# Optimization experiments

Hardware: AMD Instinct MI355X
Metric: run time of the kernel (lower is better)

## Reference

```python
import jax, jax.numpy as jnp
import numpy as np

V = 32000   # target_vocab_size
E = 512     # embedding_dim
L = 2       # enc_lstm_layers
HD = 512    # enc_lstm_hidden_dim (bidirectional encoder)
H = 2 * HD  # decoder LSTM hidden size
B = 16
T = 128
BOS = 1
CTX = L * 2 * HD          # stepwise context dim = 2048
IN0 = E + CTX             # decoder LSTM layer-0 input dim = 2560


def setup_inputs() -> dict:
    key = jax.random.key(0)
    ks = jax.random.split(key, 12)
    def w(k, shape, fan_in):
        return jax.random.normal(k, shape, jnp.float32) * np.float32(1.0 / np.sqrt(fan_in))
    return {
        "enc_lstm_hidden": jax.random.normal(ks[0], (2 * L, B, HD), jnp.float32),
        "enc_lstm_ctxt": jax.random.normal(ks[1], (2 * L, B, HD), jnp.float32),
        "minibatch_target": jax.random.randint(ks[2], (B, T), 0, V, dtype=jnp.int32),
        "emb": w(ks[3], (V, E), E),
        "w_ih_0": w(ks[4], (4 * H, IN0), IN0),
        "w_hh_0": w(ks[5], (4 * H, H), H),
        "b_ih_0": jnp.zeros((4 * H,), jnp.float32),
        "b_hh_0": jnp.zeros((4 * H,), jnp.float32),
        "w_ih_1": w(ks[6], (4 * H, H), H),
        "w_hh_1": w(ks[7], (4 * H, H), H),
        "b_ih_1": jnp.zeros((4 * H,), jnp.float32),
        "b_hh_1": jnp.zeros((4 * H,), jnp.float32),
        "fc_w": w(ks[8], (V, H), H),
        "fc_b": jnp.zeros((V,), jnp.float32),
    }


def _lstm_layer(x_seq, h0, c0, w_ih, w_hh, b):
    """x_seq: [T, B, in]; returns top outputs [T, B, H]. torch gate order i,f,g,o."""
    def step(carry, x):
        h, c = carry
        g = x @ w_ih.T + h @ w_hh.T + b
        i, f, gg, o = jnp.split(g, 4, axis=-1)
        c = jax.nn.sigmoid(f) * c + jax.nn.sigmoid(i) * jnp.tanh(gg)
        h = jax.nn.sigmoid(o) * jnp.tanh(c)
        return (h, c), h
    (hT, cT), ys = jax.lax.scan(step, (h0, c0), x_seq)
    return ys, hT, cT


def reference(enc_lstm_hidden, enc_lstm_ctxt, minibatch_target, emb,
              w_ih_0, w_hh_0, b_ih_0, b_hh_0,
              w_ih_1, w_hh_1, b_ih_1, b_hh_1, fc_w, fc_b):
    # _reshape_encoder_state: [2L,B,HD] -> [L,B,2HD] (interleave fwd/bwd per layer)
    def reshape_state(s):
        return s.reshape(L, 2, B, HD).transpose(0, 2, 1, 3).reshape(L, B, 2 * HD)
    h0 = reshape_state(enc_lstm_hidden)
    c0 = reshape_state(enc_lstm_ctxt)
    # stepwise input context: [B, 2L*HD]
    ctx = jnp.transpose(enc_lstm_hidden, (1, 0, 2)).reshape(B, CTX)
    # teacher forcing: prev tokens = [BOS, target[:, :-1]]
    tokens = jnp.concatenate(
        [jnp.full((B, 1), BOS, minibatch_target.dtype), minibatch_target[:, :-1]], axis=1)
    tok_emb = emb[tokens]                                   # [B,T,E]
    ctx_b = jnp.broadcast_to(ctx[:, None, :], (B, T, CTX))  # [B,T,CTX]
    x = jnp.concatenate([tok_emb, ctx_b], axis=-1).transpose(1, 0, 2)  # [T,B,IN0]
    x, _, _ = _lstm_layer(x, h0[0], c0[0], w_ih_0, w_hh_0, b_ih_0 + b_hh_0)
    x, _, _ = _lstm_layer(x, h0[1], c0[1], w_ih_1, w_hh_1, b_ih_1 + b_hh_1)
    out = jnp.tanh(x)                                       # [T,B,H]
    logits = jnp.einsum('tbh,vh->btv', out, fc_w) + fc_b    # [B,T,V]
    return logits
```

## Files before the change

### kernel.cpp

```cpp
#include <hip/hip_runtime.h>


#define NBLK 128

typedef float f32x4 __attribute__((ext_vector_type(4)));
typedef __bf16 bf16x8 __attribute__((ext_vector_type(8)));
typedef unsigned short u16;

__device__ __forceinline__ float sigf(float x) { return 1.0f / (1.0f + __expf(-x)); }
__device__ __forceinline__ float tanh_(float x) {
  x = fminf(15.0f, fmaxf(-15.0f, x));
  float e = __expf(2.0f * x);
  return (e - 1.0f) / (e + 1.0f);
}

__device__ __forceinline__ u16 f2bf(float f) {
  __bf16 h = (__bf16)f;
  return __builtin_bit_cast(u16, h);
}

__device__ __forceinline__ bf16x8 cvt8(float4 a, float4 b) {
  bf16x8 v;
  v[0] = (__bf16)a.x; v[1] = (__bf16)a.y; v[2] = (__bf16)a.z; v[3] = (__bf16)a.w;
  v[4] = (__bf16)b.x; v[5] = (__bf16)b.y; v[6] = (__bf16)b.z; v[7] = (__bf16)b.w;
  return v;
}

__device__ __forceinline__ void st_cv16(u16* p, u16 v) {
  unsigned vv = v;
  asm volatile("global_store_short %0, %1, off sc0 sc1" :: "v"(p), "v"(vv) : "memory");
}

__device__ __forceinline__ void flag_store(unsigned* p, unsigned v) {
  asm volatile("global_store_dword %0, %1, off sc0 sc1" :: "v"(p), "v"(v) : "memory");
}

__device__ __forceinline__ void ld2_flags(const unsigned* p0, const unsigned* p1,
                                          unsigned& a, unsigned& b) {
  asm volatile(
      "global_load_dword %0, %2, off sc0 sc1\n\t"
      "global_load_dword %1, %3, off sc0 sc1\n\t"
      "s_waitcnt vmcnt(0)"
      : "=&v"(a), "=&v"(b)
      : "v"(p0), "v"(p1)
      : "memory");
}

__device__ __forceinline__ void gsyncf(unsigned step, unsigned* bar) {
  asm volatile("s_waitcnt vmcnt(0)" ::: "memory");
  __syncthreads();
  const int tid = threadIdx.x;
  if (tid == 0) flag_store(bar + 32 + blockIdx.x * 32, step);
  if (tid < 64) {
    const unsigned* p0 = bar + 32 + tid * 64;
    const unsigned* p1 = p0 + 32;
    for (;;) {
      unsigned a, b;
      ld2_flags(p0, p1, a, b);
      if (__all((a >= step) & (b >= step))) break;
      __builtin_amdgcn_s_sleep(1);
    }
    asm volatile("" ::: "memory");
  }
  __syncthreads();
}

__device__ __forceinline__ void dot4(float& a, float4 wv, float4 xv) {
  a = fmaf(wv.x, xv.x, a);
  a = fmaf(wv.y, xv.y, a);
  a = fmaf(wv.z, xv.z, a);
  a = fmaf(wv.w, xv.w, a);
}

__global__ void prep_bf16(const float* __restrict__ src, u16* __restrict__ dst, int n8) {
  for (int i = blockIdx.x * blockDim.x + threadIdx.x; i < n8; i += gridDim.x * blockDim.x) {
    float4 a = *(const float4*)(src + (size_t)i * 8);
    float4 b = *(const float4*)(src + (size_t)i * 8 + 4);
    bf16x8 v = cvt8(a, b);
    *(uint4*)(dst + (size_t)i * 8) = __builtin_bit_cast(uint4, v);
  }
}

__global__ void prep_emb(const int* __restrict__ tgt, const float* __restrict__ emb,
                         u16* __restrict__ x0b) {
  const int g = blockIdx.x * blockDim.x + threadIdx.x;
  const int col8 = (g & 63) * 8;
  const int tb = g >> 6;
  const int t = tb >> 4, b = tb & 15;
  const int tok = (t == 0) ? 1 : tgt[b * 128 + (t - 1)];
  const float* s = emb + (size_t)tok * 512 + col8;
  float4 a = *(const float4*)s;
  float4 bb = *(const float4*)(s + 4);
  bf16x8 v = cvt8(a, bb);
  *(uint4*)(x0b + (size_t)tb * 512 + col8) = __builtin_bit_cast(uint4, v);
}

__global__ __launch_bounds__(256, 1) void prep_ctx2(const float* __restrict__ enc_h,
                                                    const float* __restrict__ wih0,
                                                    float* __restrict__ cp) {
  __shared__ float ctx[16][2052];
  const int tid = threadIdx.x;
#pragma unroll
  for (int c = 0; c < 32; ++c) {
    int f4 = tid + c * 256;
    int b = f4 >> 9, kq = f4 & 511;
    *(float4*)&ctx[b][kq * 4] =
        *(const float4*)(enc_h + (kq >> 7) * 8192 + b * 512 + (kq & 127) * 4);
  }
  __syncthreads();
  const int r = tid >> 4, l = tid & 15;
  const int j = blockIdx.x * 16 + r;
  const float* w = wih0 + (size_t)j * 2560 + 512;
  float acc[16] = {};
#pragma unroll 4
  for (int i = 0; i < 32; ++i) {
    const int k = l * 4 + i * 64;
    const float4 w4 = *(const float4*)(w + k);
#pragma unroll
    for (int b = 0; b < 16; ++b) dot4(acc[b], w4, *(const float4*)&ctx[b][k]);
  }
#pragma unroll
  for (int off = 1; off < 16; off <<= 1)
#pragma unroll
    for (int b = 0; b < 16; ++b) acc[b] += __shfl_xor(acc[b], off);
  cp[(size_t)j * 16 + l] = acc[l];
}

#define BURST(ACC, BP, S, XOFF, BW)                                            \
  _Pragma("unroll")                                                            \
  for (int mm = 0; mm < 16; ++mm) {                                            \
    bf16x8 av = *(const bf16x8*)&(BP)[fr * (S) + (XOFF) + mm * 32 + ks8];      \
    ACC = __builtin_amdgcn_mfma_f32_16x16x32_bf16(av, (BW)[mm], ACC, 0, 0, 0); \
  }

__device__ __forceinline__ void loadw(bf16x8* dst, int q, int w8, int lane,
                                      const float* wih0, const float* whh0,
                                      const float* wih1, const float* whh1) {
  const int c = q >> 1, tile = q & 1;
  const int nn = lane & 15;
  const int gate = tile * 2 + (nn >> 3);
  const int unit = nn & 7;
  const int j = gate * 1024 + w8 + unit;
  const float* src;
  size_t stride = 1024;
  int ko = 0;
  if (c == 0) { src = wih0; stride = 2560; ko = 0; }
  else if (c <= 2) { src = whh0; ko = (c - 1) * 512; }
  else if (c <= 4) { src = wih1; ko = (c - 3) * 512; }
  else { src = whh1; ko = (c - 5) * 512; }
  const float* base = src + (size_t)j * stride + ko + ((lane >> 4) * 8);
#pragma unroll
  for (int mm = 0; mm < 16; ++mm) {
    const float* sp = base + mm * 32;
    dst[mm] = cvt8(*(const float4*)sp, *(const float4*)(sp + 4));
  }
}

__global__ __launch_bounds__(512, 2) void dec_seq_rw2(
    const float* __restrict__ enc_h, const float* __restrict__ enc_c,
    const float* __restrict__ wih0, const float* __restrict__ whh0,
    const float* __restrict__ wih1, const float* __restrict__ whh1,
    const float* __restrict__ bih0, const float* __restrict__ bhh0,
    const float* __restrict__ bih1, const float* __restrict__ bhh1,
    const float* __restrict__ cp, const u16* __restrict__ x0b,
    u16* __restrict__ xr, u16* __restrict__ h1r,
    u16* __restrict__ out2b, unsigned* bar) {
  __shared__ u16 xe[16 * 520];
  __shared__ u16 xs[16 * 1032];
  __shared__ u16 h1s[16 * 1032];
  __shared__ float gls[14][16][17];

  const int tid = threadIdx.x;
  const int wgid = blockIdx.x;
  const int w8 = wgid * 8;
  const int lane = tid & 63;
  const int wave = tid >> 6;
  const int fr = lane & 15;
  const int ks8 = (lane >> 4) * 8;
  unsigned step = 0;

  bf16x8 bw0[16], bw1[16];
  const int q0 = (wave < 6) ? 2 * wave : (wave == 6 ? 12 : 13);
  loadw(bw0, q0, w8, lane, wih0, whh0, wih1, whh1);
  if (wave < 6) loadw(bw1, 2 * wave + 1, w8, lane, wih0, whh0, wih1, whh1);
  else {
#pragma unroll
    for (int mm = 0; mm < 16; ++mm) bw1[mm] = bf16x8{};
  }

  const int gdj = (tid >> 4) & 7;
  const int gb = tid & 15;
  float cpA0 = 0.f, cpA1 = 0.f, cpA2 = 0.f, cpA3 = 0.f;
  float cpB0 = 0.f, cpB1 = 0.f, cpB2 = 0.f, cpB3 = 0.f;
  float c0r = 0.f, c1r = 0.f;
  if (tid < 128) {
    const int jp = w8 + gdj;
    cpA0 = cp[(size_t)(jp) * 16 + gb] + bih0[jp] + bhh0[jp];
    cpA1 = cp[(size_t)(1024 + jp) * 16 + gb] + bih0[1024 + jp] + bhh0[1024 + jp];
    cpA2 = cp[(size_t)(2048 + jp) * 16 + gb] + bih0[2048 + jp] + bhh0[2048 + jp];
    cpA3 = cp[(size_t)(3072 + jp) * 16 + gb] + bih0[3072 + jp] + bhh0[3072 + jp];
    cpB0 = bih1[jp] + bhh1[jp];
    cpB1 = bih1[1024 + jp] + bhh1[1024 + jp];
    cpB2 = bih1[2048 + jp] + bhh1[2048 + jp];
    cpB3 = bih1[3072 + jp] + bhh1[3072 + jp];
    const int dir = jp >> 9, e = jp & 511;
    c0r = enc_c[dir * 8192 + gb * 512 + e];
    c1r = enc_c[(2 + dir) * 8192 + gb * 512 + e];
    st_cv16(xr + gb * 1024 + jp, f2bf(enc_h[dir * 8192 + gb * 512 + e]));
    st_cv16(h1r + gb * 1024 + jp, f2bf(enc_h[(2 + dir) * 8192 + gb * 512 + e]));
  }

  const int sm = tid >> 5;
  const int skq = (tid & 31) * 8;

  {
    const u16* se = x0b + sm * 512;
#pragma unroll
    for (int jj = 0; jj < 2; ++jj)
      *(uint4*)&xe[sm * 520 + skq + jj * 256] = *(const uint4*)(se + skq + jj * 256);
  }
  gsyncf(++step, bar);

  for (int s = 0; s < 129; ++s) {
    const bool doA = (s < 128), doB = (s >= 1);

    uint4 rx[4], rh[4] = {}, re[2] = {};
    {
      const u16* sx = xr + (size_t)s * 16384 + sm * 1024;
#pragma unroll
      for (int jj = 0; jj < 4; ++jj) rx[jj] = *(const uint4*)(sx + skq + jj * 256);
      if (doB) {
        const u16* sh = h1r + (size_t)(s - 1) * 16384 + sm * 1024;
#pragma unroll
        for (int jj = 0; jj < 4; ++jj) rh[jj] = *(const uint4*)(sh + skq + jj * 256);
      }
      if (s < 127) {
        const u16* se = x0b + (size_t)(s + 1) * 8192 + sm * 512;
#pragma unroll
        for (int jj = 0; jj < 2; ++jj) re[jj] = *(const uint4*)(se + skq + jj * 256);
      }
    }
#pragma unroll
    for (int jj = 0; jj < 4; ++jj) *(uint4*)&xs[sm * 1032 + skq + jj * 256] = rx[jj];
    if (doB) {
#pragma unroll
      for (int jj = 0; jj < 4; ++jj) *(uint4*)&h1s[sm * 1032 + skq + jj * 256] = rh[jj];
    }
    __syncthreads();

    f32x4 acc0 = {0.f, 0.f, 0.f, 0.f}, acc1 = {0.f, 0.f, 0.f, 0.f};
    bool act0 = false, act1 = false;
    if (wave == 0) { if (doA) { BURST(acc0, xe, 520, 0, bw0) BURST(acc1, xe, 520, 0, bw1) act0 = act1 = true; } }
    else if (wave == 1) { if (doA) { BURST(acc0, xs, 1032, 0, bw0) BURST(acc1, xs, 1032, 0, bw1) act0 = act1 = true; } }
    else if (wave == 2) { if (doA) { BURST(acc0, xs, 1032, 512, bw0) BURST(acc1, xs, 1032, 512, bw1) act0 = act1 = true; } }
    else if (wave == 3) { if (doB) { BURST(acc0, xs, 1032, 0, bw0) BURST(acc1, xs, 1032, 0, bw1) act0 = act1 = true; } }
    else if (wave == 4) { if (doB) { BURST(acc0, xs, 1032, 512, bw0) BURST(acc1, xs, 1032, 512, bw1) act0 = act1 = true; } }
    else if (wave == 5) { if (doB) { BURST(acc0, h1s, 1032, 0, bw0) BURST(acc1, h1s, 1032, 0, bw1) act0 = act1 = true; } }
    else if (wave == 6) { if (doB) { BURST(acc0, h1s, 1032, 512, bw0) act0 = true; } }
    else { if (doB) { BURST(acc0, h1s, 1032, 512, bw0) act0 = true; } }
    if (act0) {
#pragma unroll
      for (int r = 0; r < 4; ++r) gls[q0][fr][(lane >> 4) * 4 + r] = acc0[r];
    }
    if (act1) {
#pragma unroll
      for (int r = 0; r < 4; ++r) gls[q0 + 1][fr][(lane >> 4) * 4 + r] = acc1[r];
    }
    __syncthreads();

    if (s < 127) {
#pragma unroll
      for (int jj = 0; jj < 2; ++jj) *(uint4*)&xe[sm * 520 + skq + jj * 256] = re[jj];
    }

    if (tid < 128) {
      const int jp = w8 + gdj;
      if (doA) {
        float gi = gls[0][gdj][gb] + gls[2][gdj][gb] + gls[4][gdj][gb] + cpA0;
        float gf = gls[0][8 + gdj][gb] + gls[2][8 + gdj][gb] + gls[4][8 + gdj][gb] + cpA1;
        float gg = gls[1][gdj][gb] + gls[3][gdj][gb] + gls[5][gdj][gb] + cpA2;
        float go = gls[1][8 + gdj][gb] + gls[3][8 + gdj][gb] + gls[5][8 + gdj][gb] + cpA3;
        c0r = sigf(gf) * c0r + sigf(gi) * tanh_(gg);
        float h = sigf(go) * tanh_(c0r);
        st_cv16(xr + (size_t)(s + 1) * 16384 + gb * 1024 + jp, f2bf(h));
      }
      if (doB) {
        float gi = gls[6][gdj][gb] + gls[8][gdj][gb] + gls[10][gdj][gb] +
                   gls[12][gdj][gb] + cpB0;
        float gf = gls[6][8 + gdj][gb] + gls[8][8 + gdj][gb] + gls[10][8 + gdj][gb] +
                   gls[12][8 + gdj][gb] + cpB1;
        float gg = gls[7][gdj][gb] + gls[9][gdj][gb] + gls[11][gdj][gb] +
                   gls[13][gdj][gb] + cpB2;
        float go = gls[7][8 + gdj][gb] + gls[9][8 + gdj][gb] + gls[11][8 + gdj][gb] +
                   gls[13][8 + gdj][gb] + cpB3;
        c1r = sigf(gf) * c1r + sigf(gi) * tanh_(gg);
        float h = sigf(go) * tanh_(c1r);
        st_cv16(h1r + (size_t)s * 16384 + gb * 1024 + jp, f2bf(h));
        out2b[((s - 1) * 16 + gb) * 1024 + jp] = f2bf(tanh_(h));
      }
    }
    gsyncf(++step, bar);
  }
}

__global__ __launch_bounds__(256, 2) void fc_gemm_bf(
    const u16* __restrict__ A, const u16* __restrict__ Bwb,
    const float* __restrict__ bias, float* __restrict__ C) {
  __shared__ __align__(16) u16 Al[128][40];
  __shared__ __align__(16) u16 Bl[128][40];

  const int tid = threadIdx.x;
  const int m0 = blockIdx.x * 128;
  const int n0 = blockIdx.y * 128;
  const int wave = tid >> 6;
  const int lane = tid & 63;
  const int wm = (wave & 1) * 64;
  const int wn = (wave >> 1) * 64;
  const int fr = lane & 15;
  const int ks = lane >> 4;
  const int srow = tid >> 1;
  const int sh16 = (tid & 1) * 16;

  const u16* Ag = A + (size_t)(m0 + srow) * 1024 + sh16;
  const u16* Bg = Bwb + (size_t)(n0 + srow) * 1024 + sh16;

  f32x4 acc[4][4] = {};

  for (int k0 = 0; k0 < 1024; k0 += 32) {
    uint4 a0 = *(const uint4*)(Ag + k0);
    uint4 a1 = *(const uint4*)(Ag + k0 + 8);
    uint4 b0 = *(const uint4*)(Bg + k0);
    uint4 b1 = *(const uint4*)(Bg + k0 + 8);

    __syncthreads();
    *(uint4*)&Al[srow][sh16] = a0;
    *(uint4*)&Al[srow][sh16 + 8] = a1;
    *(uint4*)&Bl[srow][sh16] = b0;
    *(uint4*)&Bl[srow][sh16 + 8] = b1;
    __syncthreads();

    bf16x8 af[4], bf[4];
#pragma unroll
    for (int i = 0; i < 4; ++i) af[i] = *(const bf16x8*)&Al[wm + i * 16 + fr][ks * 8];
#pragma unroll
    for (int j = 0; j < 4; ++j) bf[j] = *(const bf16x8*)&Bl[wn + j * 16 + fr][ks * 8];
#pragma unroll
    for (int i = 0; i < 4; ++i)
#pragma unroll
      for (int j = 0; j < 4; ++j)
        acc[i][j] = __builtin_amdgcn_mfma_f32_16x16x32_bf16(af[i], bf[j], acc[i][j], 0, 0, 0);
  }

  float bj[4];
#pragma unroll
  for (int j = 0; j < 4; ++j) bj[j] = bias[n0 + wn + j * 16 + fr];

  const int mrb = (lane >> 4) * 4;
#pragma unroll
  for (int i = 0; i < 4; ++i) {
#pragma unroll
    for (int r = 0; r < 4; ++r) {
      const int m = m0 + wm + i * 16 + mrb + r;
      float* dst = C + ((size_t)(m & 15) * 128 + (m >> 4)) * 32000;
#pragma unroll
      for (int j = 0; j < 4; ++j) {
        dst[n0 + wn + j * 16 + fr] = acc[i][j][r] + bj[j];
      }
    }
  }
}

__global__ __launch_bounds__(256, 2) void fc_gemm_mfma(
    const u16* __restrict__ A, const float* __restrict__ Bw,
    const float* __restrict__ bias, float* __restrict__ C) {
  __shared__ __align__(16) u16 Al[128][40];
  __shared__ __align__(16) u16 Bl[128][40];
  const int tid = threadIdx.x;
  const int m0 = blockIdx.x * 128;
  const int n0 = blockIdx.y * 128;
  const int wave = tid >> 6;
  const int lane = tid & 63;
  const int wm = (wave & 1) * 64;
  const int wn = (wave >> 1) * 64;
  const int fr = lane & 15;
  const int ks = lane >> 4;
  const int srow = tid >> 1;
  const int sh16 = (tid & 1) * 16;
  const u16* Ag = A + (size_t)(m0 + srow) * 1024 + sh16;
  const float* Bg = Bw + (size_t)(n0 + srow) * 1024 + sh16;
  f32x4 acc[4][4] = {};
  for (int k0 = 0; k0 < 1024; k0 += 32) {
    uint4 a0 = *(const uint4*)(Ag + k0);
    uint4 a1 = *(const uint4*)(Ag + k0 + 8);
    float bfv[16];
    *(float4*)&bfv[0] = *(const float4*)(Bg + k0);
    *(float4*)&bfv[4] = *(const float4*)(Bg + k0 + 4);
    *(float4*)&bfv[8] = *(const float4*)(Bg + k0 + 8);
    *(float4*)&bfv[12] = *(const float4*)(Bg + k0 + 12);
    u16 bu[16];
#pragma unroll
    for (int u = 0; u < 16; ++u) bu[u] = f2bf(bfv[u]);
    __syncthreads();
    *(uint4*)&Al[srow][sh16] = a0;
    *(uint4*)&Al[srow][sh16 + 8] = a1;
    *(uint4*)&Bl[srow][sh16] = *(uint4*)&bu[0];
    *(uint4*)&Bl[srow][sh16 + 8] = *(uint4*)&bu[8];
    __syncthreads();
    bf16x8 af[4], bf[4];
#pragma unroll
    for (int i = 0; i < 4; ++i) af[i] = *(const bf16x8*)&Al[wm + i * 16 + fr][ks * 8];
#pragma unroll
    for (int j = 0; j < 4; ++j) bf[j] = *(const bf16x8*)&Bl[wn + j * 16 + fr][ks * 8];
#pragma unroll
    for (int i = 0; i < 4; ++i)
#pragma unroll
      for (int j = 0; j < 4; ++j)
        acc[i][j] = __builtin_amdgcn_mfma_f32_16x16x32_bf16(af[i], bf[j], acc[i][j], 0, 0, 0);
  }
  float bj[4];
#pragma unroll
  for (int j = 0; j < 4; ++j) bj[j] = bias[n0 + wn + j * 16 + fr];
  const int mrb = (lane >> 4) * 4;
#pragma unroll
  for (int i = 0; i < 4; ++i) {
#pragma unroll
    for (int r = 0; r < 4; ++r) {
      const int m = m0 + wm + i * 16 + mrb + r;
      float* dst = C + ((size_t)(m & 15) * 128 + (m >> 4)) * 32000;
#pragma unroll
      for (int j = 0; j < 4; ++j) dst[n0 + wn + j * 16 + fr] = acc[i][j][r] + bj[j];
    }
  }
}

extern "C" void kernel_launch(void* const* d_in, const int* in_sizes, int n_in,
                              void* d_out, int out_size, void* d_ws, size_t ws_size,
                              hipStream_t stream) {
  const float* enc_h = (const float*)d_in[0];
  const float* enc_c = (const float*)d_in[1];
  const int* tgt = (const int*)d_in[2];
  const float* emb = (const float*)d_in[3];
  const float* wih0 = (const float*)d_in[4];
  const float* whh0 = (const float*)d_in[5];
  const float* bih0 = (const float*)d_in[6];
  const float* bhh0 = (const float*)d_in[7];
  const float* wih1 = (const float*)d_in[8];
  const float* whh1 = (const float*)d_in[9];
  const float* bih1 = (const float*)d_in[10];
  const float* bhh1 = (const float*)d_in[11];
  const float* fcw = (const float*)d_in[12];
  const float* fcb = (const float*)d_in[13];
  float* logits = (float*)d_out;

  unsigned* bar = (unsigned*)d_ws;
  hipMemsetAsync(d_ws, 0, 32768, stream);

  float* cp = (float*)((char*)d_ws + 32768);
  u16* x0b = (u16*)(cp + 65536);
  u16* xr = x0b + 1048576;
  u16* h1r = xr + 2113536;
  u16* out2b = h1r + 2113536;
  u16* fcwb = out2b + 2097152;
  const bool use_bf_fc = (ws_size >= 80576512ull);

  prep_emb<<<512, 256, 0, stream>>>(tgt, emb, x0b);
  prep_ctx2<<<256, 256, 0, stream>>>(enc_h, wih0, cp);
  if (use_bf_fc)
    prep_bf16<<<2048, 256, 0, stream>>>(fcw, fcwb, 4096000);
  dec_seq_rw2<<<NBLK, 512, 0, stream>>>(enc_h, enc_c, wih0, whh0, wih1, whh1,
                                        bih0, bhh0, bih1, bhh1, cp, x0b,
                                        xr, h1r, out2b, bar);
  if (use_bf_fc)
    fc_gemm_bf<<<dim3(16, 250), 256, 0, stream>>>(out2b, fcwb, fcb, logits);
  else
    fc_gemm_mfma<<<dim3(16, 250), 256, 0, stream>>>(out2b, fcw, fcb, logits);
}
```

Baseline: 990.5 us.

## Replace per-step grid barrier with sentinel-polled dataflow synchronization

The per-timestep global flag barrier in the recurrent decoder is removed. Instead the xr and h1r state buffers are pre-filled with 0xFFFF sentinels, and each block polls its needed hidden-state rows with cache-bypassing loads until no sentinel remains. Blocks then proceed as soon as their own inputs are ready rather than waiting for every block, which is meant to cut barrier latency across the 129 sequential steps. In exchange it adds a memset of about 8 MB of state. Correctness now relies on a real bf16 value never equalling 0xFFFF and on the cross-block ordering of the stores.

```diff
diff --git a/kernel.cpp b/kernel.cpp
--- a/kernel.cpp
+++ b/kernel.cpp
@@ -31,38 +31,34 @@
   asm volatile("global_store_short %0, %1, off sc0 sc1" :: "v"(p), "v"(vv) : "memory");
 }
 
-__device__ __forceinline__ void flag_store(unsigned* p, unsigned v) {
-  asm volatile("global_store_dword %0, %1, off sc0 sc1" :: "v"(p), "v"(v) : "memory");
-}
-
-__device__ __forceinline__ void ld2_flags(const unsigned* p0, const unsigned* p1,
-                                          unsigned& a, unsigned& b) {
+__device__ __forceinline__ void ld8x16_cv(
+    const u16* a0, const u16* a1, const u16* a2, const u16* a3,
+    const u16* a4, const u16* a5, const u16* a6, const u16* a7,
+    uint4& v0, uint4& v1, uint4& v2, uint4& v3,
+    uint4& v4, uint4& v5, uint4& v6, uint4& v7) {
   asm volatile(
-      "global_load_dword %0, %2, off sc0 sc1\n\t"
-      "global_load_dword %1, %3, off sc0 sc1\n\t"
+      "global_load_dwordx4 %0, %8, off sc0 sc1\n\t"
+      "global_load_dwordx4 %1, %9, off sc0 sc1\n\t"
+      "global_load_dwordx4 %2, %10, off sc0 sc1\n\t"
+      "global_load_dwordx4 %3, %11, off sc0 sc1\n\t"
+      "global_load_dwordx4 %4, %12, off sc0 sc1\n\t"
+      "global_load_dwordx4 %5, %13, off sc0 sc1\n\t"
+      "global_load_dwordx4 %6, %14, off sc0 sc1\n\t"
+      "global_load_dwordx4 %7, %15, off sc0 sc1\n\t"
       "s_waitcnt vmcnt(0)"
-      : "=&v"(a), "=&v"(b)
-      : "v"(p0), "v"(p1)
+      : "=&v"(v0), "=&v"(v1), "=&v"(v2), "=&v"(v3),
+        "=&v"(v4), "=&v"(v5), "=&v"(v6), "=&v"(v7)
+      : "v"(a0), "v"(a1), "v"(a2), "v"(a3), "v"(a4), "v"(a5), "v"(a6), "v"(a7)
       : "memory");
 }
 
-__device__ __forceinline__ void gsyncf(unsigned step, unsigned* bar) {
-  asm volatile("s_waitcnt vmcnt(0)" ::: "memory");
-  __syncthreads();
-  const int tid = threadIdx.x;
-  if (tid == 0) flag_store(bar + 32 + blockIdx.x * 32, step);
-  if (tid < 64) {
-    const unsigned* p0 = bar + 32 + tid * 64;
-    const unsigned* p1 = p0 + 32;
-    for (;;) {
-      unsigned a, b;
-      ld2_flags(p0, p1, a, b);
-      if (__all((a >= step) & (b >= step))) break;
-      __builtin_amdgcn_s_sleep(1);
-    }
-    asm volatile("" ::: "memory");
-  }
-  __syncthreads();
+__device__ __forceinline__ bool ok16(uint4 v) {
+  unsigned bad = 0;
+  bad |= ((v.x & 0xFFFFu) == 0xFFFFu); bad |= ((v.x >> 16) == 0xFFFFu);
+  bad |= ((v.y & 0xFFFFu) == 0xFFFFu); bad |= ((v.y >> 16) == 0xFFFFu);
+  bad |= ((v.z & 0xFFFFu) == 0xFFFFu); bad |= ((v.z >> 16) == 0xFFFFu);
+  bad |= ((v.w & 0xFFFFu) == 0xFFFFu); bad |= ((v.w >> 16) == 0xFFFFu);
+  return bad == 0;
 }
 
 __device__ __forceinline__ void dot4(float& a, float4 wv, float4 xv) {
@@ -156,7 +152,7 @@
   }
 }
 
-__global__ __launch_bounds__(512, 2) void dec_seq_rw2(
+__global__ __launch_bounds__(512, 2) void dec_seq_df(
     const float* __restrict__ enc_h, const float* __restrict__ enc_c,
     const float* __restrict__ wih0, const float* __restrict__ whh0,
     const float* __restrict__ wih1, const float* __restrict__ whh1,
@@ -164,7 +160,7 @@
     const float* __restrict__ bih1, const float* __restrict__ bhh1,
     const float* __restrict__ cp, const u16* __restrict__ x0b,
     u16* __restrict__ xr, u16* __restrict__ h1r,
-    u16* __restrict__ out2b, unsigned* bar) {
+    u16* __restrict__ out2b) {
   __shared__ u16 xe[16 * 520];
   __shared__ u16 xs[16 * 1032];
   __shared__ u16 h1s[16 * 1032];
@@ -177,7 +173,6 @@
   const int wave = tid >> 6;
   const int fr = lane & 15;
   const int ks8 = (lane >> 4) * 8;
-  unsigned step = 0;
 
   bf16x8 bw0[16], bw1[16];
   const int q0 = (wave < 6) ? 2 * wave : (wave == 6 ? 12 : 13);
@@ -219,32 +214,37 @@
     for (int jj = 0; jj < 2; ++jj)
       *(uint4*)&xe[sm * 520 + skq + jj * 256] = *(const uint4*)(se + skq + jj * 256);
   }
-  gsyncf(++step, bar);
 
   for (int s = 0; s < 129; ++s) {
     const bool doA = (s < 128), doB = (s >= 1);
 
-    uint4 rx[4], rh[4] = {}, re[2] = {};
-    {
-      const u16* sx = xr + (size_t)s * 16384 + sm * 1024;
-#pragma unroll
-      for (int jj = 0; jj < 4; ++jj) rx[jj] = *(const uint4*)(sx + skq + jj * 256);
-      if (doB) {
-        const u16* sh = h1r + (size_t)(s - 1) * 16384 + sm * 1024;
-#pragma unroll
-        for (int jj = 0; jj < 4; ++jj) rh[jj] = *(const uint4*)(sh + skq + jj * 256);
-      }
-      if (s < 127) {
-        const u16* se = x0b + (size_t)(s + 1) * 8192 + sm * 512;
-#pragma unroll
-        for (int jj = 0; jj < 2; ++jj) re[jj] = *(const uint4*)(se + skq + jj * 256);
-      }
-    }
-#pragma unroll
-    for (int jj = 0; jj < 4; ++jj) *(uint4*)&xs[sm * 1032 + skq + jj * 256] = rx[jj];
+    uint4 re[2] = {};
+    if (s < 127) {
+      const u16* se = x0b + (size_t)(s + 1) * 8192 + sm * 512;
+#pragma unroll
+      for (int jj = 0; jj < 2; ++jj) re[jj] = *(const uint4*)(se + skq + jj * 256);
+    }
+
+    const u16* sx = xr + (size_t)s * 16384 + sm * 1024 + skq;
+    const u16* sh = h1r + (size_t)(doB ? (s - 1) : 0) * 16384 + sm * 1024 + skq;
+    uint4 X0, X1, X2, X3, H0, H1, H2, H3;
+    for (;;) {
+      ld8x16_cv(sx, sx + 256, sx + 512, sx + 768, sh, sh + 256, sh + 512, sh + 768,
+                X0, X1, X2, X3, H0, H1, H2, H3);
+      bool ok = ok16(X0) & ok16(X1) & ok16(X2) & ok16(X3);
+      if (doB) ok = ok & ok16(H0) & ok16(H1) & ok16(H2) & ok16(H3);
+      if (ok) break;
+      __builtin_amdgcn_s_sleep(1);
+    }
+    *(uint4*)&xs[sm * 1032 + skq] = X0;
+    *(uint4*)&xs[sm * 1032 + skq + 256] = X1;
+    *(uint4*)&xs[sm * 1032 + skq + 512] = X2;
+    *(uint4*)&xs[sm * 1032 + skq + 768] = X3;
     if (doB) {
-#pragma unroll
-      for (int jj = 0; jj < 4; ++jj) *(uint4*)&h1s[sm * 1032 + skq + jj * 256] = rh[jj];
+      *(uint4*)&h1s[sm * 1032 + skq] = H0;
+      *(uint4*)&h1s[sm * 1032 + skq + 256] = H1;
+      *(uint4*)&h1s[sm * 1032 + skq + 512] = H2;
+      *(uint4*)&h1s[sm * 1032 + skq + 768] = H3;
     }
     __syncthreads();
 
@@ -299,7 +299,6 @@
         out2b[((s - 1) * 16 + gb) * 1024 + jp] = f2bf(tanh_(h));
       }
     }
-    gsyncf(++step, bar);
   }
 }
 
@@ -452,9 +451,6 @@
   const float* fcb = (const float*)d_in[13];
   float* logits = (float*)d_out;
 
-  unsigned* bar = (unsigned*)d_ws;
-  hipMemsetAsync(d_ws, 0, 32768, stream);
-
   float* cp = (float*)((char*)d_ws + 32768);
   u16* x0b = (u16*)(cp + 65536);
   u16* xr = x0b + 1048576;
@@ -463,13 +459,15 @@
   u16* fcwb = out2b + 2097152;
   const bool use_bf_fc = (ws_size >= 80576512ull);
 
+  hipMemsetAsync(xr, 0xFF, 2 * 2113536 * sizeof(u16), stream);
+
   prep_emb<<<512, 256, 0, stream>>>(tgt, emb, x0b);
   prep_ctx2<<<256, 256, 0, stream>>>(enc_h, wih0, cp);
   if (use_bf_fc)
     prep_bf16<<<2048, 256, 0, stream>>>(fcw, fcwb, 4096000);
-  dec_seq_rw2<<<NBLK, 512, 0, stream>>>(enc_h, enc_c, wih0, whh0, wih1, whh1,
-                                        bih0, bhh0, bih1, bhh1, cp, x0b,
-                                        xr, h1r, out2b, bar);
+  dec_seq_df<<<NBLK, 512, 0, stream>>>(enc_h, enc_c, wih0, whh0, wih1, whh1,
+                                       bih0, bhh0, bih1, bhh1, cp, x0b,
+                                       xr, h1r, out2b);
   if (use_bf_fc)
     fc_gemm_bf<<<dim3(16, 250), 256, 0, stream>>>(out2b, fcwb, fcb, logits);
   else
```

Measured after the change: 1.433 ms. 44.7% more time.

## Fuse FC projection into persistent decoder kernel, overlapping with recurrence via flags

Applied to the files above, without the earlier changes.

Merges the decoder recurrence and the vocabulary projection into one persistent launch. 128 blocks run the LSTM steps while 125 extra blocks convert their slice of fc_w to bf16 and then compute logits for each 128-row chunk as soon as the step flags show those rows of out2b are written. This hides the FC GEMM and the weight conversion behind the latency-bound serial recurrence and removes two kernel launches. The risks are that the FC blocks' polling and memory traffic slow the step barrier, and that launch_bounds drops to 1 block per CU with a large shared-memory footprint, which assumes all 253 blocks are resident at once.

```diff
diff --git a/kernel.cpp b/kernel.cpp
--- a/kernel.cpp
+++ b/kernel.cpp
@@ -2,6 +2,7 @@
 
 
 #define NBLK 128
+#define NFCB 125
 
 typedef float f32x4 __attribute__((ext_vector_type(4)));
 typedef __bf16 bf16x8 __attribute__((ext_vector_type(8)));
@@ -44,6 +45,13 @@
       : "=&v"(a), "=&v"(b)
       : "v"(p0), "v"(p1)
       : "memory");
+}
+
+__device__ __forceinline__ void ld1_cv(const u16* p, uint4& v) {
+  asm volatile(
+      "global_load_dwordx4 %0, %1, off sc0 sc1\n\t"
+      "s_waitcnt vmcnt(0)"
+      : "=&v"(v) : "v"(p) : "memory");
 }
 
 __device__ __forceinline__ void gsyncf(unsigned step, unsigned* bar) {
@@ -65,20 +73,27 @@
   __syncthreads();
 }
 
+__device__ __forceinline__ void wait_flags(unsigned target, const unsigned* bar) {
+  const int tid = threadIdx.x;
+  if (tid < 64) {
+    const unsigned* p0 = bar + 32 + tid * 64;
+    const unsigned* p1 = p0 + 32;
+    for (;;) {
+      unsigned a, b;
+      ld2_flags(p0, p1, a, b);
+      if (__all((a >= target) & (b >= target))) break;
+      __builtin_amdgcn_s_sleep(4);
+    }
+    asm volatile("" ::: "memory");
+  }
+  __syncthreads();
+}
+
 __device__ __forceinline__ void dot4(float& a, float4 wv, float4 xv) {
   a = fmaf(wv.x, xv.x, a);
   a = fmaf(wv.y, xv.y, a);
   a = fmaf(wv.z, xv.z, a);
   a = fmaf(wv.w, xv.w, a);
-}
-
-__global__ void prep_bf16(const float* __restrict__ src, u16* __restrict__ dst, int n8) {
-  for (int i = blockIdx.x * blockDim.x + threadIdx.x; i < n8; i += gridDim.x * blockDim.x) {
-    float4 a = *(const float4*)(src + (size_t)i * 8);
-    float4 b = *(const float4*)(src + (size_t)i * 8 + 4);
-    bf16x8 v = cvt8(a, b);
-    *(uint4*)(dst + (size_t)i * 8) = __builtin_bit_cast(uint4, v);
-  }
 }
 
 __global__ void prep_emb(const int* __restrict__ tgt, const float* __restrict__ emb,
@@ -156,215 +171,222 @@
   }
 }
 
-__global__ __launch_bounds__(512, 2) void dec_seq_rw2(
+__global__ __launch_bounds__(512, 1) void dec_fc(
     const float* __restrict__ enc_h, const float* __restrict__ enc_c,
     const float* __restrict__ wih0, const float* __restrict__ whh0,
     const float* __restrict__ wih1, const float* __restrict__ whh1,
     const float* __restrict__ bih0, const float* __restrict__ bhh0,
     const float* __restrict__ bih1, const float* __restrict__ bhh1,
     const float* __restrict__ cp, const u16* __restrict__ x0b,
-    u16* __restrict__ xr, u16* __restrict__ h1r,
-    u16* __restrict__ out2b, unsigned* bar) {
-  __shared__ u16 xe[16 * 520];
-  __shared__ u16 xs[16 * 1032];
-  __shared__ u16 h1s[16 * 1032];
-  __shared__ float gls[14][16][17];
+    u16* __restrict__ xr, u16* __restrict__ h1r, u16* __restrict__ out2b,
+    const float* __restrict__ fcw, const float* __restrict__ fcb,
+    u16* __restrict__ fcwb, float* __restrict__ logits, unsigned* bar) {
+  __shared__ __align__(16) char smem[97920];
 
   const int tid = threadIdx.x;
   const int wgid = blockIdx.x;
-  const int w8 = wgid * 8;
   const int lane = tid & 63;
   const int wave = tid >> 6;
   const int fr = lane & 15;
   const int ks8 = (lane >> 4) * 8;
-  unsigned step = 0;
-
-  bf16x8 bw0[16], bw1[16];
-  const int q0 = (wave < 6) ? 2 * wave : (wave == 6 ? 12 : 13);
-  loadw(bw0, q0, w8, lane, wih0, whh0, wih1, whh1);
-  if (wave < 6) loadw(bw1, 2 * wave + 1, w8, lane, wih0, whh0, wih1, whh1);
-  else {
-#pragma unroll
-    for (int mm = 0; mm < 16; ++mm) bw1[mm] = bf16x8{};
-  }
-
-  const int gdj = (tid >> 4) & 7;
-  const int gb = tid & 15;
-  float cpA0 = 0.f, cpA1 = 0.f, cpA2 = 0.f, cpA3 = 0.f;
-  float cpB0 = 0.f, cpB1 = 0.f, cpB2 = 0.f, cpB3 = 0.f;
-  float c0r = 0.f, c1r = 0.f;
-  if (tid < 128) {
-    const int jp = w8 + gdj;
-    cpA0 = cp[(size_t)(jp) * 16 + gb] + bih0[jp] + bhh0[jp];
-    cpA1 = cp[(size_t)(1024 + jp) * 16 + gb] + bih0[1024 + jp] + bhh0[1024 + jp];
-    cpA2 = cp[(size_t)(2048 + jp) * 16 + gb] + bih0[2048 + jp] + bhh0[2048 + jp];
-    cpA3 = cp[(size_t)(3072 + jp) * 16 + gb] + bih0[3072 + jp] + bhh0[3072 + jp];
-    cpB0 = bih1[jp] + bhh1[jp];
-    cpB1 = bih1[1024 + jp] + bhh1[1024 + jp];
-    cpB2 = bih1[2048 + jp] + bhh1[2048 + jp];
-    cpB3 = bih1[3072 + jp] + bhh1[3072 + jp];
-    const int dir = jp >> 9, e = jp & 511;
-    c0r = enc_c[dir * 8192 + gb * 512 + e];
-    c1r = enc_c[(2 + dir) * 8192 + gb * 512 + e];
-    st_cv16(xr + gb * 1024 + jp, f2bf(enc_h[dir * 8192 + gb * 512 + e]));
-    st_cv16(h1r + gb * 1024 + jp, f2bf(enc_h[(2 + dir) * 8192 + gb * 512 + e]));
-  }
-
-  const int sm = tid >> 5;
-  const int skq = (tid & 31) * 8;
-
-  {
-    const u16* se = x0b + sm * 512;
-#pragma unroll
-    for (int jj = 0; jj < 2; ++jj)
-      *(uint4*)&xe[sm * 520 + skq + jj * 256] = *(const uint4*)(se + skq + jj * 256);
-  }
-  gsyncf(++step, bar);
-
-  for (int s = 0; s < 129; ++s) {
-    const bool doA = (s < 128), doB = (s >= 1);
-
-    uint4 rx[4], rh[4] = {}, re[2] = {};
-    {
-      const u16* sx = xr + (size_t)s * 16384 + sm * 1024;
-#pragma unroll
-      for (int jj = 0; jj < 4; ++jj) rx[jj] = *(const uint4*)(sx + skq + jj * 256);
-      if (doB) {
-        const u16* sh = h1r + (size_t)(s - 1) * 16384 + sm * 1024;
-#pragma unroll
-        for (int jj = 0; jj < 4; ++jj) rh[jj] = *(const uint4*)(sh + skq + jj * 256);
-      }
-      if (s < 127) {
-        const u16* se = x0b + (size_t)(s + 1) * 8192 + sm * 512;
-#pragma unroll
-        for (int jj = 0; jj < 2; ++jj) re[jj] = *(const uint4*)(se + skq + jj * 256);
-      }
-    }
-#pragma unroll
-    for (int jj = 0; jj < 4; ++jj) *(uint4*)&xs[sm * 1032 + skq + jj * 256] = rx[jj];
-    if (doB) {
-#pragma unroll
-      for (int jj = 0; jj < 4; ++jj) *(uint4*)&h1s[sm * 1032 + skq + jj * 256] = rh[jj];
-    }
-    __syncthreads();
-
-    f32x4 acc0 = {0.f, 0.f, 0.f, 0.f}, acc1 = {0.f, 0.f, 0.f, 0.f};
-    bool act0 = false, act1 = false;
-    if (wave == 0) { if (doA) { BURST(acc0, xe, 520, 0, bw0) BURST(acc1, xe, 520, 0, bw1) act0 = act1 = true; } }
-    else if (wave == 1) { if (doA) { BURST(acc0, xs, 1032, 0, bw0) BURST(acc1, xs, 1032, 0, bw1) act0 = act1 = true; } }
-    else if (wave == 2) { if (doA) { BURST(acc0, xs, 1032, 512, bw0) BURST(acc1, xs, 1032, 512, bw1) act0 = act1 = true; } }
-    else if (wave == 3) { if (doB) { BURST(acc0, xs, 1032, 0, bw0) BURST(acc1, xs, 1032, 0, bw1) act0 = act1 = true; } }
-    else if (wave == 4) { if (doB) { BURST(acc0, xs, 1032, 512, bw0) BURST(acc1, xs, 1032, 512, bw1) act0 = act1 = true; } }
-    else if (wave == 5) { if (doB) { BURST(acc0, h1s, 1032, 0, bw0) BURST(acc1, h1s, 1032, 0, bw1) act0 = act1 = true; } }
-    else if (wave == 6) { if (doB) { BURST(acc0, h1s, 1032, 512, bw0) act0 = true; } }
-    else { if (doB) { BURST(acc0, h1s, 1032, 512, bw0) act0 = true; } }
-    if (act0) {
-#pragma unroll
-      for (int r = 0; r < 4; ++r) gls[q0][fr][(lane >> 4) * 4 + r] = acc0[r];
-    }
-    if (act1) {
-#pragma unroll
-      for (int r = 0; r < 4; ++r) gls[q0 + 1][fr][(lane >> 4) * 4 + r] = acc1[r];
-    }
-    __syncthreads();
-
-    if (s < 127) {
-#pragma unroll
-      for (int jj = 0; jj < 2; ++jj) *(uint4*)&xe[sm * 520 + skq + jj * 256] = re[jj];
-    }
-
+
+  if (wgid < NBLK) {
+    u16* xe = (u16*)smem;
+    u16* xs = xe + 16 * 520;
+    u16* h1s = xs + 16 * 1032;
+    float (*gls)[16][17] = (float(*)[16][17])(h1s + 16 * 1032);
+
+    const int w8 = wgid * 8;
+    unsigned step = 0;
+
+    bf16x8 bw0[16], bw1[16];
+    const int q0 = (wave < 6) ? 2 * wave : (wave == 6 ? 12 : 13);
+    loadw(bw0, q0, w8, lane, wih0, whh0, wih1, whh1);
+    if (wave < 6) loadw(bw1, 2 * wave + 1, w8, lane, wih0, whh0, wih1, whh1);
+    else {
+#pragma unroll
+      for (int mm = 0; mm < 16; ++mm) bw1[mm] = bf16x8{};
+    }
+
+    const int gdj = (tid >> 4) & 7;
+    const int gb = tid & 15;
+    float cpA0 = 0.f, cpA1 = 0.f, cpA2 = 0.f, cpA3 = 0.f;
+    float cpB0 = 0.f, cpB1 = 0.f, cpB2 = 0.f, cpB3 = 0.f;
+    float c0r = 0.f, c1r = 0.f;
     if (tid < 128) {
       const int jp = w8 + gdj;
-      if (doA) {
-        float gi = gls[0][gdj][gb] + gls[2][gdj][gb] + gls[4][gdj][gb] + cpA0;
-        float gf = gls[0][8 + gdj][gb] + gls[2][8 + gdj][gb] + gls[4][8 + gdj][gb] + cpA1;
-        float gg = gls[1][gdj][gb] + gls[3][gdj][gb] + gls[5][gdj][gb] + cpA2;
-        float go = gls[1][8 + gdj][gb] + gls[3][8 + gdj][gb] + gls[5][8 + gdj][gb] + cpA3;
-        c0r = sigf(gf) * c0r + sigf(gi) * tanh_(gg);
-        float h = sigf(go) * tanh_(c0r);
-        st_cv16(xr + (size_t)(s + 1) * 16384 + gb * 1024 + jp, f2bf(h));
-      }
+      cpA0 = cp[(size_t)(jp) * 16 + gb] + bih0[jp] + bhh0[jp];
+      cpA1 = cp[(size_t)(1024 + jp) * 16 + gb] + bih0[1024 + jp] + bhh0[1024 + jp];
+      cpA2 = cp[(size_t)(2048 + jp) * 16 + gb] + bih0[2048 + jp] + bhh0[2048 + jp];
+      cpA3 = cp[(size_t)(3072 + jp) * 16 + gb] + bih0[3072 + jp] + bhh0[3072 + jp];
+      cpB0 = bih1[jp] + bhh1[jp];
+      cpB1 = bih1[1024 + jp] + bhh1[1024 + jp];
+      cpB2 = bih1[2048 + jp] + bhh1[2048 + jp];
+      cpB3 = bih1[3072 + jp] + bhh1[3072 + jp];
+      const int dir = jp >> 9, e = jp & 511;
+      c0r = enc_c[dir * 8192 + gb * 512 + e];
+      c1r = enc_c[(2 + dir) * 8192 + gb * 512 + e];
+      st_cv16(xr + gb * 1024 + jp, f2bf(enc_h[dir * 8192 + gb * 512 + e]));
+      st_cv16(h1r + gb * 1024 + jp, f2bf(enc_h[(2 + dir) * 8192 + gb * 512 + e]));
+    }
+
+    const int sm = tid >> 5;
+    const int skq = (tid & 31) * 8;
+
+    {
+      const u16* se = x0b + sm * 512;
+#pragma unroll
+      for (int jj = 0; jj < 2; ++jj)
+        *(uint4*)&xe[sm * 520 + skq + jj * 256] = *(const uint4*)(se + skq + jj * 256);
+    }
+    gsyncf(++step, bar);
+
+    for (int s = 0; s < 129; ++s) {
+      const bool doA = (s < 128), doB = (s >= 1);
+
+      uint4 rx[4], rh[4] = {}, re[2] = {};
+      {
+        const u16* sx = xr + (size_t)s * 16384 + sm * 1024;
+#pragma unroll
+        for (int jj = 0; jj < 4; ++jj) rx[jj] = *(const uint4*)(sx + skq + jj * 256);
+        if (doB) {
+          const u16* sh = h1r + (size_t)(s - 1) * 16384 + sm * 1024;
+#pragma unroll
+          for (int jj = 0; jj < 4; ++jj) rh[jj] = *(const uint4*)(sh + skq + jj * 256);
+        }
+        if (s < 127) {
+          const u16* se = x0b + (size_t)(s + 1) * 8192 + sm * 512;
+#pragma unroll
+          for (int jj = 0; jj < 2; ++jj) re[jj] = *(const uint4*)(se + skq + jj * 256);
+        }
+      }
+#pragma unroll
+      for (int jj = 0; jj < 4; ++jj) *(uint4*)&xs[sm * 1032 + skq + jj * 256] = rx[jj];
       if (doB) {
-        float gi = gls[6][gdj][gb] + gls[8][gdj][gb] + gls[10][gdj][gb] +
-                   gls[12][gdj][gb] + cpB0;
-        float gf = gls[6][8 + gdj][gb] + gls[8][8 + gdj][gb] + gls[10][8 + gdj][gb] +
-                   gls[12][8 + gdj][gb] + cpB1;
-        float gg = gls[7][gdj][gb] + gls[9][gdj][gb] + gls[11][gdj][gb] +
-                   gls[13][gdj][gb] + cpB2;
-        float go = gls[7][8 + gdj][gb] + gls[9][8 + gdj][gb] + gls[11][8 + gdj][gb] +
-                   gls[13][8 + gdj][gb] + cpB3;
-        c1r = sigf(gf) * c1r + sigf(gi) * tanh_(gg);
-        float h = sigf(go) * tanh_(c1r);
-        st_cv16(h1r + (size_t)s * 16384 + gb * 1024 + jp, f2bf(h));
-        out2b[((s - 1) * 16 + gb) * 1024 + jp] = f2bf(tanh_(h));
-      }
-    }
-    gsyncf(++step, bar);
-  }
-}
-
-__global__ __launch_bounds__(256, 2) void fc_gemm_bf(
-    const u16* __restrict__ A, const u16* __restrict__ Bwb,
-    const float* __restrict__ bias, float* __restrict__ C) {
-  __shared__ __align__(16) u16 Al[128][40];
-  __shared__ __align__(16) u16 Bl[128][40];
-
-  const int tid = threadIdx.x;
-  const int m0 = blockIdx.x * 128;
-  const int n0 = blockIdx.y * 128;
-  const int wave = tid >> 6;
-  const int lane = tid & 63;
-  const int wm = (wave & 1) * 64;
-  const int wn = (wave >> 1) * 64;
-  const int fr = lane & 15;
-  const int ks = lane >> 4;
-  const int srow = tid >> 1;
-  const int sh16 = (tid & 1) * 16;
-
-  const u16* Ag = A + (size_t)(m0 + srow) * 1024 + sh16;
-  const u16* Bg = Bwb + (size_t)(n0 + srow) * 1024 + sh16;
-
-  f32x4 acc[4][4] = {};
-
-  for (int k0 = 0; k0 < 1024; k0 += 32) {
-    uint4 a0 = *(const uint4*)(Ag + k0);
-    uint4 a1 = *(const uint4*)(Ag + k0 + 8);
-    uint4 b0 = *(const uint4*)(Bg + k0);
-    uint4 b1 = *(const uint4*)(Bg + k0 + 8);
-
+#pragma unroll
+        for (int jj = 0; jj < 4; ++jj) *(uint4*)&h1s[sm * 1032 + skq + jj * 256] = rh[jj];
+      }
+      __syncthreads();
+
+      f32x4 acc0 = {0.f, 0.f, 0.f, 0.f}, acc1 = {0.f, 0.f, 0.f, 0.f};
+      bool act0 = false, act1 = false;
+      if (wave == 0) { if (doA) { BURST(acc0, xe, 520, 0, bw0) BURST(acc1, xe, 520, 0, bw1) act0 = act1 = true; } }
+      else if (wave == 1) { if (doA) { BURST(acc0, xs, 1032, 0, bw0) BURST(acc1, xs, 1032, 0, bw1) act0 = act1 = true; } }
+      else if (wave == 2) { if (doA) { BURST(acc0, xs, 1032, 512, bw0) BURST(acc1, xs, 1032, 512, bw1) act0 = act1 = true; } }
+      else if (wave == 3) { if (doB) { BURST(acc0, xs, 1032, 0, bw0) BURST(acc1, xs, 1032, 0, bw1) act0 = act1 = true; } }
+      else if (wave == 4) { if (doB) { BURST(acc0, xs, 1032, 512, bw0) BURST(acc1, xs, 1032, 512, bw1) act0 = act1 = true; } }
+      else if (wave == 5) { if (doB) { BURST(acc0, h1s, 1032, 0, bw0) BURST(acc1, h1s, 1032, 0, bw1) act0 = act1 = true; } }
+      else if (wave == 6) { if (doB) { BURST(acc0, h1s, 1032, 512, bw0) act0 = true; } }
+      else { if (doB) { BURST(acc0, h1s, 1032, 512, bw0) act0 = true; } }
+      if (act0) {
+#pragma unroll
+        for (int r = 0; r < 4; ++r) gls[q0][fr][(lane >> 4) * 4 + r] = acc0[r];
+      }
+      if (act1) {
+#pragma unroll
+        for (int r = 0; r < 4; ++r) gls[q0 + 1][fr][(lane >> 4) * 4 + r] = acc1[r];
+      }
+      __syncthreads();
+
+      if (s < 127) {
+#pragma unroll
+        for (int jj = 0; jj < 2; ++jj) *(uint4*)&xe[sm * 520 + skq + jj * 256] = re[jj];
+      }
+
+      if (tid < 128) {
+        const int jp = w8 + gdj;
+        if (doA) {
+          float gi = gls[0][gdj][gb] + gls[2][gdj][gb] + gls[4][gdj][gb] + cpA0;
+          float gf = gls[0][8 + gdj][gb] + gls[2][8 + gdj][gb] + gls[4][8 + gdj][gb] + cpA1;
+          float gg = gls[1][gdj][gb] + gls[3][gdj][gb] + gls[5][gdj][gb] + cpA2;
+          float go = gls[1][8 + gdj][gb] + gls[3][8 + gdj][gb] + gls[5][8 + gdj][gb] + cpA3;
+          c0r = sigf(gf) * c0r + sigf(gi) * tanh_(gg);
+          float h = sigf(go) * tanh_(c0r);
+          st_cv16(xr + (size_t)(s + 1) * 16384 + gb * 1024 + jp, f2bf(h));
+        }
+        if (doB) {
+          float gi = gls[6][gdj][gb] + gls[8][gdj][gb] + gls[10][gdj][gb] +
+                     gls[12][gdj][gb] + cpB0;
+          float gf = gls[6][8 + gdj][gb] + gls[8][8 + gdj][gb] + gls[10][8 + gdj][gb] +
+                     gls[12][8 + gdj][gb] + cpB1;
+          float gg = gls[7][gdj][gb] + gls[9][gdj][gb] + gls[11][gdj][gb] +
+                     gls[13][gdj][gb] + cpB2;
+          float go = gls[7][8 + gdj][gb] + gls[9][8 + gdj][gb] + gls[11][8 + gdj][gb] +
+                     gls[13][8 + gdj][gb] + cpB3;
+          c1r = sigf(gf) * c1r + sigf(gi) * tanh_(gg);
+          float h = sigf(go) * tanh_(c1r);
+          st_cv16(h1r + (size_t)s * 16384 + gb * 1024 + jp, f2bf(h));
+          st_cv16(out2b + ((s - 1) * 16 + gb) * 1024 + jp, f2bf(tanh_(h)));
+        }
+      }
+      gsyncf(++step, bar);
+    }
+  } else {
+    u16 (*Al)[40] = (u16(*)[40])smem;
+    u16 (*Bl)[40] = (u16(*)[40])(smem + 10240);
+
+    const int fb = wgid - NBLK;
+    const int n0 = fb * 256;
+
+    for (int i = tid; i < 32768; i += 512) {
+      const int row = i >> 7;
+      const int c8 = (i & 127) * 8;
+      const float* s = fcw + (size_t)(n0 + row) * 1024 + c8;
+      bf16x8 v = cvt8(*(const float4*)s, *(const float4*)(s + 4));
+      *(uint4*)(fcwb + (size_t)(n0 + row) * 1024 + c8) = __builtin_bit_cast(uint4, v);
+    }
     __syncthreads();
-    *(uint4*)&Al[srow][sh16] = a0;
-    *(uint4*)&Al[srow][sh16 + 8] = a1;
-    *(uint4*)&Bl[srow][sh16] = b0;
-    *(uint4*)&Bl[srow][sh16 + 8] = b1;
-    __syncthreads();
-
-    bf16x8 af[4], bf[4];
-#pragma unroll
-    for (int i = 0; i < 4; ++i) af[i] = *(const bf16x8*)&Al[wm + i * 16 + fr][ks * 8];
-#pragma unroll
-    for (int j = 0; j < 4; ++j) bf[j] = *(const bf16x8*)&Bl[wn + j * 16 + fr][ks * 8];
-#pragma unroll
-    for (int i = 0; i < 4; ++i)
-#pragma unroll
-      for (int j = 0; j < 4; ++j)
-        acc[i][j] = __builtin_amdgcn_mfma_f32_16x16x32_bf16(af[i], bf[j], acc[i][j], 0, 0, 0);
-  }
-
-  float bj[4];
-#pragma unroll
-  for (int j = 0; j < 4; ++j) bj[j] = bias[n0 + wn + j * 16 + fr];
-
-  const int mrb = (lane >> 4) * 4;
-#pragma unroll
-  for (int i = 0; i < 4; ++i) {
-#pragma unroll
-    for (int r = 0; r < 4; ++r) {
-      const int m = m0 + wm + i * 16 + mrb + r;
-      float* dst = C + ((size_t)(m & 15) * 128 + (m >> 4)) * 32000;
-#pragma unroll
-      for (int j = 0; j < 4; ++j) {
-        dst[n0 + wn + j * 16 + fr] = acc[i][j][r] + bj[j];
+
+    const int wm = (wave & 1) * 64;
+    const int wn = (wave >> 1) * 64;
+    float bj[4];
+#pragma unroll
+    for (int j = 0; j < 4; ++j) bj[j] = fcb[n0 + wn + j * 16 + fr];
+
+    const int rA = tid >> 2, cA = (tid & 3) * 8;
+    const int rB = tid >> 1, cB = (tid & 1) * 16;
+    const u16* Bs = fcwb + (size_t)(n0 + rB) * 1024 + cB;
+    const int mrb = (lane >> 4) * 4;
+
+    for (int m0 = 0; m0 < 16; ++m0) {
+      wait_flags((unsigned)(m0 * 8 + 10), bar);
+
+      f32x4 acc[4][4] = {};
+      const u16* Ag = out2b + (size_t)(m0 * 128 + rA) * 1024 + cA;
+      for (int k0 = 0; k0 < 1024; k0 += 32) {
+        uint4 av;
+        ld1_cv(Ag + k0, av);
+        uint4 b0 = *(const uint4*)(Bs + k0);
+        uint4 b1 = *(const uint4*)(Bs + k0 + 8);
+        __syncthreads();
+        *(uint4*)&Al[rA][cA] = av;
+        *(uint4*)&Bl[rB][cB] = b0;
+        *(uint4*)&Bl[rB][cB + 8] = b1;
+        __syncthreads();
+
+        bf16x8 af[4], bf[4];
+#pragma unroll
+        for (int i = 0; i < 4; ++i) af[i] = *(const bf16x8*)&Al[wm + i * 16 + fr][ks8];
+#pragma unroll
+        for (int j = 0; j < 4; ++j) bf[j] = *(const bf16x8*)&Bl[wn + j * 16 + fr][ks8];
+#pragma unroll
+        for (int i = 0; i < 4; ++i)
+#pragma unroll
+          for (int j = 0; j < 4; ++j)
+            acc[i][j] = __builtin_amdgcn_mfma_f32_16x16x32_bf16(af[i], bf[j], acc[i][j], 0, 0, 0);
+      }
+
+#pragma unroll
+      for (int i = 0; i < 4; ++i) {
+#pragma unroll
+        for (int r = 0; r < 4; ++r) {
+          const int m = m0 * 128 + wm + i * 16 + mrb + r;
+          float* dst = logits + ((size_t)(m & 15) * 128 + (m >> 4)) * 32000;
+#pragma unroll
+          for (int j = 0; j < 4; ++j) {
+            dst[n0 + wn + j * 16 + fr] = acc[i][j][r] + bj[j];
+          }
+        }
       }
     }
   }
@@ -461,17 +483,20 @@
   u16* h1r = xr + 2113536;
   u16* out2b = h1r + 2113536;
   u16* fcwb = out2b + 2097152;
-  const bool use_bf_fc = (ws_size >= 80576512ull);
+  const bool fused = (ws_size >= 80576512ull);
 
   prep_emb<<<512, 256, 0, stream>>>(tgt, emb, x0b);
   prep_ctx2<<<256, 256, 0, stream>>>(enc_h, wih0, cp);
-  if (use_bf_fc)
-    prep_bf16<<<2048, 256, 0, stream>>>(fcw, fcwb, 4096000);
-  dec_seq_rw2<<<NBLK, 512, 0, stream>>>(enc_h, enc_c, wih0, whh0, wih1, whh1,
-                                        bih0, bhh0, bih1, bhh1, cp, x0b,
-                                        xr, h1r, out2b, bar);
-  if (use_bf_fc)
-    fc_gemm_bf<<<dim3(16, 250), 256, 0, stream>>>(out2b, fcwb, fcb, logits);
-  else
+  if (fused) {
+    dec_fc<<<NBLK + NFCB, 512, 0, stream>>>(enc_h, enc_c, wih0, whh0, wih1, whh1,
+                                            bih0, bhh0, bih1, bhh1, cp, x0b,
+                                            xr, h1r, out2b, fcw, fcb, fcwb,
+                                            logits, bar);
+  } else {
+    dec_fc<<<NBLK, 512, 0, stream>>>(enc_h, enc_c, wih0, whh0, wih1, whh1,
+                                     bih0, bhh0, bih1, bhh1, cp, x0b,
+                                     xr, h1r, out2b, fcw, fcb, fcwb,
+                                     logits, bar);
     fc_gemm_mfma<<<dim3(16, 250), 256, 0, stream>>>(out2b, fcw, fcb, logits);
-}
+  }
+}
```

After: 986.7 us. Within noise of the previous version (-0.4%).
